# Kernel optimization log

Measured on AMD Instinct MI355X. Metric: run time of the kernel, lower is better.

The kernel has to match this reference:

```python
import jax, jax.numpy as jnp
import numpy as np

B, S, D, H, WINDOW = 2, 2048, 2048, 16, 256
HD = D // H  # head_dim = 128

def setup_inputs() -> dict:
    key = jax.random.key(0)
    ks = jax.random.split(key, 6)
    s = 0.02  # initializer_range-like scale for weights
    return {
        "hidden_states": jax.random.normal(ks[0], (B, S, D), jnp.float32),
        "attention_mask": jnp.ones((B, S), jnp.int32),
        "Wq": jax.random.normal(ks[1], (D, D), jnp.float32) * s,
        "Wk": jax.random.normal(ks[2], (D, D), jnp.float32) * s,
        "Wv": jax.random.normal(ks[3], (D, D), jnp.float32) * s,
        "Wo": jax.random.normal(ks[4], (D, D), jnp.float32) * s,
        "bo": jnp.zeros((D,), jnp.float32),
    }

def reference(hidden_states, attention_mask, Wq, Wk, Wv, Wo, bo):
    # GPT-Neo quirk: query is multiplied by sqrt(head_dim) and then
    # dot_product_attention_weights divides by sqrt(head_dim) -> net UNSCALED scores.
    q = (hidden_states @ Wq).reshape(B, S, H, HD)  # [B,S,H,hd]
    k = (hidden_states @ Wk).reshape(B, S, H, HD)
    v = (hidden_states @ Wv).reshape(B, S, H, HD)

    # local causal mask: attend iff i - window < j <= i
    i = jnp.arange(S)[:, None]
    j = jnp.arange(S)[None, :]
    local_causal = (j <= i) & (j > i - WINDOW)  # [S,S]
    mask = local_causal[None, None] & (attention_mask[:, None, None, :] > 0)  # [B,1,S,S]

    neg = jnp.finfo(jnp.float32).min
    scores = jnp.einsum("bqhd,bkhd->bhqk", q, k)  # [B,H,S,S] unscaled
    scores = jnp.where(mask, scores, neg)
    attn = jax.nn.softmax(scores, axis=-1)

    out = jnp.einsum("bhqk,bkhd->bqhd", attn, v).reshape(B, S, D)
    return out @ Wo + bo
```

## Files before the change

kernel.cpp:

```cpp
#include <hip/hip_runtime.h>

#define B_   2
#define S_   2048
#define D_   2048
#define H_   16
#define HD_  128
#define WIN_ 256
#define M_   (B_ * S_)

typedef float  f32x4  __attribute__((ext_vector_type(4)));
typedef short  s16x8  __attribute__((ext_vector_type(8)));
typedef __bf16 bf16x8 __attribute__((ext_vector_type(8)));
typedef unsigned short ushort_t;

__device__ inline unsigned short f2b(float f) {
  unsigned u = __builtin_bit_cast(unsigned, f);
  u += 0x7fffu + ((u >> 16) & 1u);
  return (unsigned short)(u >> 16);
}
__device__ inline float b2f(unsigned short h) {
  unsigned u = ((unsigned)h) << 16;
  return __builtin_bit_cast(float, u);
}

template <typename T>
__device__ auto mfma_impl(T a, T b, f32x4 c, int)
    -> decltype(__builtin_amdgcn_mfma_f32_16x16x32_bf16(a, b, c, 0, 0, 0)) {
  return __builtin_amdgcn_mfma_f32_16x16x32_bf16(a, b, c, 0, 0, 0);
}
template <typename T>
__device__ f32x4 mfma_impl(T a, T b, f32x4 c, long) {
  return __builtin_amdgcn_mfma_f32_16x16x32_bf16(
      __builtin_bit_cast(bf16x8, a), __builtin_bit_cast(bf16x8, b), c, 0, 0, 0);
}
__device__ inline f32x4 mfma_bf16(s16x8 a, s16x8 b, f32x4 c) {
  return mfma_impl(a, b, c, 0);
}

#if defined(__has_builtin)
#if __has_builtin(__builtin_amdgcn_global_load_lds)
#define HAS_GLL 1
#endif
#endif
#ifndef HAS_GLL
#define HAS_GLL 0
#endif

__device__ inline void gl_lds16(const ushort_t* g, ushort_t* lds_wave_base) {
#if HAS_GLL
  __builtin_amdgcn_global_load_lds(
      (const __attribute__((address_space(1))) unsigned int*)g,
      (__attribute__((address_space(3))) unsigned int*)lds_wave_base, 16, 0, 0);
#else
  const int lane = threadIdx.x & 63;
  *(uint4*)(lds_wave_base + lane * 8) = *(const uint4*)g;
#endif
}

__global__ __launch_bounds__(256) void k_split(const float* __restrict__ x,
                                               ushort_t* __restrict__ hi,
                                               ushort_t* __restrict__ lo, int n) {
  int i = (blockIdx.x * 256 + threadIdx.x) * 4;
  if (i + 3 < n) {
    float4 v = *(const float4*)(x + i);
    ushort4 h, l;
    h.x = f2b(v.x); l.x = f2b(v.x - b2f(h.x));
    h.y = f2b(v.y); l.y = f2b(v.y - b2f(h.y));
    h.z = f2b(v.z); l.z = f2b(v.z - b2f(h.z));
    h.w = f2b(v.w); l.w = f2b(v.w - b2f(h.w));
    *(ushort4*)(hi + i) = h;
    *(ushort4*)(lo + i) = l;
  }
}

__global__ __launch_bounds__(256) void k_transpose4(const float* __restrict__ W0,
                                                    const float* __restrict__ W1,
                                                    const float* __restrict__ W2,
                                                    const float* __restrict__ W3,
                                                    ushort_t* __restrict__ T0h,
                                                    ushort_t* __restrict__ T0l,
                                                    ushort_t* __restrict__ T1h,
                                                    ushort_t* __restrict__ T1l,
                                                    ushort_t* __restrict__ T2h,
                                                    ushort_t* __restrict__ T3h) {
  __shared__ float t[32][33];
  const int z = blockIdx.z;
  const float* W = (z == 0) ? W0 : (z == 1) ? W1 : (z == 2) ? W2 : W3;
  ushort_t* Th = (z == 0) ? T0h : (z == 1) ? T1h : (z == 2) ? T2h : T3h;
  ushort_t* Tl = (z == 0) ? T0l : (z == 1) ? T1l : nullptr;
  int bx = blockIdx.x * 32, by = blockIdx.y * 32;
  int tx = threadIdx.x, ty = threadIdx.y;
#pragma unroll
  for (int r = 0; r < 32; r += 8)
    t[ty + r][tx] = W[(size_t)(by + ty + r) * D_ + bx + tx];
  __syncthreads();
#pragma unroll
  for (int r = 0; r < 32; r += 8) {
    float v = t[tx][ty + r];
    unsigned short h = f2b(v);
    Th[(size_t)(bx + ty + r) * D_ + by + tx] = h;
    if (Tl) Tl[(size_t)(bx + ty + r) * D_ + by + tx] = f2b(v - b2f(h));
  }
}

__global__ __launch_bounds__(256) void k_vtrans(const ushort_t* __restrict__ Vb,
                                                ushort_t* __restrict__ Vt) {
  __shared__ ushort_t t[32][33];
  int bx = blockIdx.x * 32, by = blockIdx.y * 32, b = blockIdx.z;
  int tx = threadIdx.x, ty = threadIdx.y;
#pragma unroll
  for (int r = 0; r < 32; r += 8)
    t[ty + r][tx] = Vb[((size_t)(b * S_ + by + ty + r)) * D_ + bx + tx];
  __syncthreads();
#pragma unroll
  for (int r = 0; r < 32; r += 8)
    Vt[((size_t)(b * D_ + bx + ty + r)) * S_ + by + tx] = t[tx][ty + r];
}

template <int SPLIT, int OUT>
__global__ __launch_bounds__(256) void k_gemm(const ushort_t* __restrict__ Ah,
                                              const ushort_t* __restrict__ Al,
                                              const ushort_t* __restrict__ Bh,
                                              const ushort_t* __restrict__ Bl,
                                              ushort_t* __restrict__ Co,
                                              ushort_t* __restrict__ Col,
                                              float* __restrict__ Cf,
                                              const float* __restrict__ bias,
                                              int M, int N, int K) {
  constexpr int NA = (SPLIT >= 2) ? 2 : 1;
  constexpr int NBB = (SPLIT == 3) ? 2 : 1;
  __shared__ ushort_t Ash[NA][128][32];
  __shared__ ushort_t Bsh[NBB][128][32];
  const int tid = threadIdx.x;
  const int wave = tid >> 6, lane = tid & 63;
  const int m0 = blockIdx.y * 128, n0 = blockIdx.x * 128;
  const int wr = (wave >> 1) * 64, wc = (wave & 1) * 64;
  const int quad = lane >> 4, l16 = lane & 15;
  const int srow = tid >> 2, scol = (tid & 3) * 8;
  const size_t aoff = (size_t)(m0 + srow) * K + scol;
  const size_t boff = (size_t)(n0 + srow) * K + scol;
  const int wofs = wave * 512;

  f32x4 acc[4][4] = {};
  for (int k0 = 0; k0 < K; k0 += 32) {
    gl_lds16(Ah + aoff + k0,                  &Ash[0][0][0] + wofs);
    gl_lds16(Ah + aoff + k0 + (size_t)64 * K, &Ash[0][64][0] + wofs);
    if (SPLIT >= 2) {
      gl_lds16(Al + aoff + k0,                  &Ash[NA - 1][0][0] + wofs);
      gl_lds16(Al + aoff + k0 + (size_t)64 * K, &Ash[NA - 1][64][0] + wofs);
    }
    gl_lds16(Bh + boff + k0,                  &Bsh[0][0][0] + wofs);
    gl_lds16(Bh + boff + k0 + (size_t)64 * K, &Bsh[0][64][0] + wofs);
    if (SPLIT == 3) {
      gl_lds16(Bl + boff + k0,                  &Bsh[NBB - 1][0][0] + wofs);
      gl_lds16(Bl + boff + k0 + (size_t)64 * K, &Bsh[NBB - 1][64][0] + wofs);
    }
    __syncthreads();
    s16x8 bf[NBB][4];
#pragma unroll
    for (int s = 0; s < NBB; s++)
#pragma unroll
      for (int jt = 0; jt < 4; jt++)
        bf[s][jt] = *(const s16x8*)&Bsh[s][wc + jt * 16 + l16][quad * 8];
#pragma unroll
    for (int it = 0; it < 4; it++) {
      s16x8 ah = *(const s16x8*)&Ash[0][wr + it * 16 + l16][quad * 8];
      s16x8 al;
      if (SPLIT >= 2) al = *(const s16x8*)&Ash[NA - 1][wr + it * 16 + l16][quad * 8];
#pragma unroll
      for (int jt = 0; jt < 4; jt++) {
        acc[it][jt] = mfma_bf16(ah, bf[0][jt], acc[it][jt]);
        if (SPLIT == 3)
          acc[it][jt] = mfma_bf16(ah, bf[NBB - 1][jt], acc[it][jt]);
        if (SPLIT >= 2)
          acc[it][jt] = mfma_bf16(al, bf[0][jt], acc[it][jt]);
      }
    }
    __syncthreads();
  }
#pragma unroll
  for (int it = 0; it < 4; it++)
#pragma unroll
    for (int jt = 0; jt < 4; jt++)
#pragma unroll
      for (int r = 0; r < 4; r++) {
        int row = m0 + wr + it * 16 + quad * 4 + r;
        int col = n0 + wc + jt * 16 + l16;
        float v = acc[it][jt][r];
        if (OUT == 2) {
          Cf[(size_t)row * N + col] = v + bias[col];
        } else if (OUT == 1) {
          unsigned short h = f2b(v);
          Co[(size_t)row * N + col]  = h;
          Col[(size_t)row * N + col] = f2b(v - b2f(h));
        } else {
          Co[(size_t)row * N + col] = f2b(v);
        }
      }
}

__global__ __launch_bounds__(256) void k_fattn(const ushort_t* __restrict__ Qh,
                                               const ushort_t* __restrict__ Ql,
                                               const ushort_t* __restrict__ Kh,
                                               const ushort_t* __restrict__ Vt,
                                               const int* __restrict__ amask,
                                               ushort_t* __restrict__ AO) {
  __shared__ ushort_t Ksh[64][136];
  __shared__ ushort_t Vs[128][72];
  __shared__ ushort_t ps[4][16][72];
  __shared__ int ams[320];
  const int tid = threadIdx.x;
  const int wave = tid >> 6, lane = tid & 63;
  const int quad = lane >> 4, l16 = lane & 15;
  const int qt = blockIdx.x, h = blockIdx.y, b = blockIdx.z;
  const int q0 = qt * 64;

  for (int x = tid; x < 320; x += 256) {
    int j = q0 - 256 + x;
    ams[x] = (j >= 0) ? amask[b * S_ + j] : 0;
  }

  const int qrowA = q0 + wave * 16 + l16;
  const ushort_t* qbh = Qh + ((size_t)(b * S_ + qrowA) * D_) + h * HD_;
  const ushort_t* qbl = Ql + ((size_t)(b * S_ + qrowA) * D_) + h * HD_;
  s16x8 qh[4], ql[4];
#pragma unroll
  for (int kk = 0; kk < 4; kk++) {
    qh[kk] = *(const s16x8*)(qbh + kk * 32 + quad * 8);
    ql[kk] = *(const s16x8*)(qbl + kk * 32 + quad * 8);
  }

  f32x4 O[8] = {};
  float m_run[4], l_run[4];
#pragma unroll
  for (int r = 0; r < 4; r++) { m_run[r] = -3.0e38f; l_run[r] = 0.f; }

  const int t0 = (qt < 4) ? (4 - qt) : 0;
  for (int t = t0; t < 5; t++) {
    const int kb = q0 - 256 + 64 * t;
    __syncthreads();
    {
      const int key = tid >> 2, dimb = (tid & 3) * 32;
      const ushort_t* kgh = Kh + ((size_t)(b * S_ + kb + key) * D_) + h * HD_ + dimb;
#pragma unroll
      for (int u = 0; u < 4; u++)
        *(uint4*)&Ksh[key][dimb + u * 8] = *(const uint4*)(kgh + u * 8);
      const int hd = tid >> 1, keyb = (tid & 1) * 32;
      const ushort_t* vg = Vt + ((size_t)(b * D_ + h * HD_ + hd) * S_) + kb + keyb;
#pragma unroll
      for (int u = 0; u < 4; u++)
        *(uint4*)&Vs[hd][keyb + u * 8] = *(const uint4*)(vg + u * 8);
    }
    __syncthreads();

    f32x4 sacc[4] = {};
#pragma unroll
    for (int kk = 0; kk < 4; kk++)
#pragma unroll
      for (int nt = 0; nt < 4; nt++) {
        s16x8 kfh = *(const s16x8*)&Ksh[nt * 16 + l16][kk * 32 + quad * 8];
        sacc[nt] = mfma_bf16(qh[kk], kfh, sacc[nt]);
        sacc[nt] = mfma_bf16(ql[kk], kfh, sacc[nt]);
      }

#pragma unroll
    for (int nt = 0; nt < 4; nt++) {
      const int j = kb + nt * 16 + l16;
      const bool amok = ams[64 * t + nt * 16 + l16] != 0;
#pragma unroll
      for (int r = 0; r < 4; r++) {
        const int iq = q0 + wave * 16 + quad * 4 + r;
        const bool ok = amok && (j <= iq) && (j > iq - WIN_);
        if (!ok) sacc[nt][r] = -3.0e38f;
      }
    }
    float mt[4];
#pragma unroll
    for (int r = 0; r < 4; r++) {
      mt[r] = fmaxf(fmaxf(sacc[0][r], sacc[1][r]), fmaxf(sacc[2][r], sacc[3][r]));
      mt[r] = fmaxf(mt[r], __shfl_xor(mt[r], 1));
      mt[r] = fmaxf(mt[r], __shfl_xor(mt[r], 2));
      mt[r] = fmaxf(mt[r], __shfl_xor(mt[r], 4));
      mt[r] = fmaxf(mt[r], __shfl_xor(mt[r], 8));
    }
    float alpha[4], lt[4];
#pragma unroll
    for (int r = 0; r < 4; r++) {
      float mnew = fmaxf(m_run[r], mt[r]);
      alpha[r] = __expf(m_run[r] - mnew);
      m_run[r] = mnew;
      lt[r] = 0.f;
#pragma unroll
      for (int nt = 0; nt < 4; nt++) {
        float s = sacc[nt][r];
        float p = (s > -1.0e30f) ? __expf(s - mnew) : 0.f;
        sacc[nt][r] = p;
        lt[r] += p;
      }
      lt[r] += __shfl_xor(lt[r], 1);
      lt[r] += __shfl_xor(lt[r], 2);
      lt[r] += __shfl_xor(lt[r], 4);
      lt[r] += __shfl_xor(lt[r], 8);
      l_run[r] = l_run[r] * alpha[r] + lt[r];
    }
#pragma unroll
    for (int o = 0; o < 8; o++)
#pragma unroll
      for (int r = 0; r < 4; r++) O[o][r] *= alpha[r];
#pragma unroll
    for (int nt = 0; nt < 4; nt++)
#pragma unroll
      for (int r = 0; r < 4; r++)
        ps[wave][quad * 4 + r][nt * 16 + l16] = f2b(sacc[nt][r]);
    __syncthreads();
#pragma unroll
    for (int kk2 = 0; kk2 < 2; kk2++) {
      s16x8 pf = *(const s16x8*)&ps[wave][l16][kk2 * 32 + quad * 8];
#pragma unroll
      for (int o = 0; o < 8; o++) {
        s16x8 vf = *(const s16x8*)&Vs[o * 16 + l16][kk2 * 32 + quad * 8];
        O[o] = mfma_bf16(pf, vf, O[o]);
      }
    }
  }
#pragma unroll
  for (int r = 0; r < 4; r++) l_run[r] = 1.0f / l_run[r];
#pragma unroll
  for (int o = 0; o < 8; o++)
#pragma unroll
    for (int r = 0; r < 4; r++) {
      int row = q0 + wave * 16 + quad * 4 + r;
      AO[((size_t)(b * S_ + row) * D_) + h * HD_ + o * 16 + l16] = f2b(O[o][r] * l_run[r]);
    }
}

extern "C" void kernel_launch(void* const* d_in, const int* in_sizes, int n_in,
                              void* d_out, int out_size, void* d_ws, size_t ws_size,
                              hipStream_t stream) {
  const float* hs    = (const float*)d_in[0];
  const int*   amask = (const int*)d_in[1];
  const float* Wq    = (const float*)d_in[2];
  const float* Wk    = (const float*)d_in[3];
  const float* Wv    = (const float*)d_in[4];
  const float* Wo    = (const float*)d_in[5];
  const float* bo    = (const float*)d_in[6];
  float* out = (float*)d_out;

  char* p = (char*)d_ws;
  ushort_t* hsHi = (ushort_t*)p; p += (size_t)16 << 20;
  ushort_t* hsLo = (ushort_t*)p; p += (size_t)16 << 20;
  ushort_t* WqTh = (ushort_t*)p; p += (size_t)8 << 20;
  ushort_t* WqTl = (ushort_t*)p; p += (size_t)8 << 20;
  ushort_t* WkTh = (ushort_t*)p; p += (size_t)8 << 20;
  ushort_t* WkTl = (ushort_t*)p; p += (size_t)8 << 20;  (void)WkTl;
  ushort_t* WvTh = (ushort_t*)p; p += (size_t)8 << 20;
  ushort_t* WoTh = (ushort_t*)p; p += (size_t)8 << 20;
  ushort_t* Qhb  = (ushort_t*)p; p += (size_t)16 << 20;
  ushort_t* Qlb  = (ushort_t*)p; p += (size_t)16 << 20;
  ushort_t* Khb  = (ushort_t*)p; p += (size_t)16 << 20;
  ushort_t* Vb   = (ushort_t*)p; p += (size_t)16 << 20;
  ushort_t* Vt   = (ushort_t*)p; p += (size_t)16 << 20;

  k_split<<<M_ * D_ / 1024, 256, 0, stream>>>(hs, hsHi, hsLo, M_ * D_);
  dim3 tb(32, 8), tg4(D_ / 32, D_ / 32, 4);
  k_transpose4<<<tg4, tb, 0, stream>>>(Wq, Wk, Wv, Wo, WqTh, WqTl, WkTh, nullptr, WvTh, WoTh);

  dim3 gg(D_ / 128, M_ / 128);
  k_gemm<3, 1><<<gg, 256, 0, stream>>>(hsHi, hsLo, WqTh, WqTl, Qhb, Qlb, nullptr, nullptr, M_, D_, D_);
  k_gemm<2, 0><<<gg, 256, 0, stream>>>(hsHi, hsLo, WkTh, nullptr, Khb, nullptr, nullptr, nullptr, M_, D_, D_);
  k_gemm<1, 0><<<gg, 256, 0, stream>>>(hsHi, nullptr, WvTh, nullptr, Vb, nullptr, nullptr, nullptr, M_, D_, D_);

  dim3 vg(D_ / 32, S_ / 32, B_);
  k_vtrans<<<vg, tb, 0, stream>>>(Vb, Vt);

  dim3 ag(S_ / 64, H_, B_);
  k_fattn<<<ag, 256, 0, stream>>>(Qhb, Qlb, Khb, Vt, amask, hsHi );

  k_gemm<1, 2><<<gg, 256, 0, stream>>>(hsHi , nullptr, WoTh, nullptr, nullptr, nullptr, out, bo, M_, D_, D_);
}
```

Baseline: 494.8 us.

## Replace GEMM with 256x128-tile, triple-buffered, swizzled-LDS 8-wave kernel

Replaces the 128x128, 4-wave GEMM with a 512-thread kernel that computes a 256x128 tile using a 64-wide K step. Global-to-LDS staging is triple-buffered and overlapped with MFMA work through explicit waitcnt, barriers and setprio. The LDS layout uses an XOR swizzle to avoid bank conflicts. The split-precision products are now handled as extra K segments (hi*hi, lo*hi, hi*lo) with one MFMA per term instead of interleaving them per tile. The risks are higher LDS use, which lowers occupancy, and fewer blocks in the grid.

```diff
diff --git a/kernel.cpp b/kernel.cpp
--- a/kernel.cpp
+++ b/kernel.cpp
@@ -117,76 +117,135 @@
     Vt[((size_t)(b * D_ + bx + ty + r)) * S_ + by + tx] = t[tx][ty + r];
 }
 
-template <int SPLIT, int OUT>
-__global__ __launch_bounds__(256) void k_gemm(const ushort_t* __restrict__ Ah,
-                                              const ushort_t* __restrict__ Al,
-                                              const ushort_t* __restrict__ Bh,
-                                              const ushort_t* __restrict__ Bl,
-                                              ushort_t* __restrict__ Co,
-                                              ushort_t* __restrict__ Col,
-                                              float* __restrict__ Cf,
-                                              const float* __restrict__ bias,
-                                              int M, int N, int K) {
-  constexpr int NA = (SPLIT >= 2) ? 2 : 1;
-  constexpr int NBB = (SPLIT == 3) ? 2 : 1;
-  __shared__ ushort_t Ash[NA][128][32];
-  __shared__ ushort_t Bsh[NBB][128][32];
+
+__device__ inline void stage_chunk(const ushort_t* __restrict__ gbase, int K,
+                                   int rowbase, ushort_t* ldsTile, int tid) {
+  const int rr = tid >> 3;
+  const int gs = ((tid & 7) ^ (rr & 7)) * 8;
+  gl_lds16(gbase + (size_t)(rowbase + rr) * K + gs,
+           ldsTile + rowbase * 64 + (tid >> 6) * 512);
+}
+
+template <int NSEG, int OUT>
+__global__ __launch_bounds__(512) void k_gemm8(
+    const ushort_t* __restrict__ A0, const ushort_t* __restrict__ A1,
+    const ushort_t* __restrict__ A2, const ushort_t* __restrict__ B0,
+    const ushort_t* __restrict__ B2, ushort_t* __restrict__ Co,
+    ushort_t* __restrict__ Col, float* __restrict__ Cf,
+    const float* __restrict__ bias, int M, int N, int K) {
+  __shared__ ushort_t As_[3][256 * 64];
+  __shared__ ushort_t Bs_[3][128 * 64];
   const int tid = threadIdx.x;
   const int wave = tid >> 6, lane = tid & 63;
-  const int m0 = blockIdx.y * 128, n0 = blockIdx.x * 128;
-  const int wr = (wave >> 1) * 64, wc = (wave & 1) * 64;
   const int quad = lane >> 4, l16 = lane & 15;
-  const int srow = tid >> 2, scol = (tid & 3) * 8;
-  const size_t aoff = (size_t)(m0 + srow) * K + scol;
-  const size_t boff = (size_t)(n0 + srow) * K + scol;
-  const int wofs = wave * 512;
+  const int m0 = blockIdx.y * 256, n0 = blockIdx.x * 128;
+  const int wrM = (wave >> 1) * 64;
+  const int wcN = (wave & 1) * 64;
+  const int aRowB = (wrM + l16) * 64;
+  const int bRowB = (wcN + l16) * 64;
+  int ks8[2];
+  ks8[0] = ((0 + quad) ^ (l16 & 7)) * 8;
+  ks8[1] = ((4 + quad) ^ (l16 & 7)) * 8;
+  const int NT = NSEG * 32;
+
+  {
+    const ushort_t* Ab0 = A0 + (size_t)m0 * K;
+    const ushort_t* Bb0 = B0 + (size_t)n0 * K;
+#pragma unroll
+    for (int t = 0; t < 2; ++t) {
+      const ushort_t* Ab = Ab0 + t * 64;
+      const ushort_t* Bb = Bb0 + t * 64;
+      stage_chunk(Ab, K, 0,   &As_[t][0], tid);
+      stage_chunk(Ab, K, 64,  &As_[t][0], tid);
+      stage_chunk(Ab, K, 128, &As_[t][0], tid);
+      stage_chunk(Ab, K, 192, &As_[t][0], tid);
+      stage_chunk(Bb, K, 0,   &Bs_[t][0], tid);
+      stage_chunk(Bb, K, 64,  &Bs_[t][0], tid);
+    }
+  }
+  asm volatile("s_waitcnt vmcnt(6)" ::: "memory");
+  __builtin_amdgcn_s_barrier();
+  asm volatile("" ::: "memory");
 
   f32x4 acc[4][4] = {};
-  for (int k0 = 0; k0 < K; k0 += 32) {
-    gl_lds16(Ah + aoff + k0,                  &Ash[0][0][0] + wofs);
-    gl_lds16(Ah + aoff + k0 + (size_t)64 * K, &Ash[0][64][0] + wofs);
-    if (SPLIT >= 2) {
-      gl_lds16(Al + aoff + k0,                  &Ash[NA - 1][0][0] + wofs);
-      gl_lds16(Al + aoff + k0 + (size_t)64 * K, &Ash[NA - 1][64][0] + wofs);
-    }
-    gl_lds16(Bh + boff + k0,                  &Bsh[0][0][0] + wofs);
-    gl_lds16(Bh + boff + k0 + (size_t)64 * K, &Bsh[0][64][0] + wofs);
-    if (SPLIT == 3) {
-      gl_lds16(Bl + boff + k0,                  &Bsh[NBB - 1][0][0] + wofs);
-      gl_lds16(Bl + boff + k0 + (size_t)64 * K, &Bsh[NBB - 1][64][0] + wofs);
-    }
-    __syncthreads();
-    s16x8 bf[NBB][4];
-#pragma unroll
-    for (int s = 0; s < NBB; s++)
-#pragma unroll
-      for (int jt = 0; jt < 4; jt++)
-        bf[s][jt] = *(const s16x8*)&Bsh[s][wc + jt * 16 + l16][quad * 8];
-#pragma unroll
-    for (int it = 0; it < 4; it++) {
-      s16x8 ah = *(const s16x8*)&Ash[0][wr + it * 16 + l16][quad * 8];
-      s16x8 al;
-      if (SPLIT >= 2) al = *(const s16x8*)&Ash[NA - 1][wr + it * 16 + l16][quad * 8];
-#pragma unroll
-      for (int jt = 0; jt < 4; jt++) {
-        acc[it][jt] = mfma_bf16(ah, bf[0][jt], acc[it][jt]);
-        if (SPLIT == 3)
-          acc[it][jt] = mfma_bf16(ah, bf[NBB - 1][jt], acc[it][jt]);
-        if (SPLIT >= 2)
-          acc[it][jt] = mfma_bf16(al, bf[0][jt], acc[it][jt]);
-      }
-    }
-    __syncthreads();
-  }
-#pragma unroll
-  for (int it = 0; it < 4; it++)
-#pragma unroll
-    for (int jt = 0; jt < 4; jt++)
-#pragma unroll
-      for (int r = 0; r < 4; r++) {
-        int row = m0 + wr + it * 16 + quad * 4 + r;
-        int col = n0 + wc + jt * 16 + l16;
-        float v = acc[it][jt][r];
+  int cur = 0;
+  for (int kt = 0; kt < NT; ++kt) {
+    const int st = kt + 2;
+    const bool doStage = (st < NT);
+    int sbuf = cur + 2; if (sbuf >= 3) sbuf -= 3;
+    ushort_t* At  = &As_[cur][0];
+    ushort_t* Bt  = &Bs_[cur][0];
+    ushort_t* Ads = &As_[sbuf][0];
+    ushort_t* Bds = &Bs_[sbuf][0];
+    const ushort_t* Asb = A0;
+    const ushort_t* Bsb = B0;
+    if (doStage) {
+      const int sg = st >> 5;
+      const ushort_t* Ag = A0;
+      const ushort_t* Bg = B0;
+      if (NSEG >= 2 && sg == 1) Ag = A1;
+      if (NSEG == 3 && sg == 2) { Ag = A2; Bg = B2; }
+      Asb = Ag + (size_t)m0 * K + (size_t)(st & 31) * 64;
+      Bsb = Bg + (size_t)n0 * K + (size_t)(st & 31) * 64;
+    }
+    s16x8 bf[4][2];
+#pragma unroll
+    for (int p = 0; p < 2; ++p) {
+      s16x8 af[2][2];
+#pragma unroll
+      for (int i = 0; i < 2; ++i)
+#pragma unroll
+        for (int s = 0; s < 2; ++s)
+          af[i][s] = *(const s16x8*)(At + aRowB + (p * 2 + i) * 1024 + ks8[s]);
+      if (p == 0) {
+#pragma unroll
+        for (int nt = 0; nt < 4; ++nt)
+#pragma unroll
+          for (int s = 0; s < 2; ++s)
+            bf[nt][s] = *(const s16x8*)(Bt + bRowB + nt * 1024 + ks8[s]);
+      }
+      if (doStage) {
+        if (p == 0) {
+          stage_chunk(Asb, K, 0,   Ads, tid);
+          stage_chunk(Asb, K, 64,  Ads, tid);
+          stage_chunk(Asb, K, 128, Ads, tid);
+        } else {
+          stage_chunk(Asb, K, 192, Ads, tid);
+          stage_chunk(Bsb, K, 0,   Bds, tid);
+          stage_chunk(Bsb, K, 64,  Bds, tid);
+        }
+      }
+      __builtin_amdgcn_s_barrier();
+      asm volatile("s_waitcnt lgkmcnt(0)" ::: "memory");
+      __builtin_amdgcn_sched_barrier(0);
+      __builtin_amdgcn_s_setprio(1);
+#pragma unroll
+      for (int i = 0; i < 2; ++i)
+#pragma unroll
+        for (int nt = 0; nt < 4; ++nt)
+#pragma unroll
+          for (int s = 0; s < 2; ++s)
+            acc[p * 2 + i][nt] = mfma_bf16(af[i][s], bf[nt][s], acc[p * 2 + i][nt]);
+      __builtin_amdgcn_s_setprio(0);
+      if (p == 1) {
+        if (doStage) asm volatile("s_waitcnt vmcnt(6)" ::: "memory");
+        else         asm volatile("s_waitcnt vmcnt(0)" ::: "memory");
+      }
+      __builtin_amdgcn_s_barrier();
+      asm volatile("" ::: "memory");
+    }
+    cur = (cur == 2) ? 0 : cur + 1;
+  }
+
+#pragma unroll
+  for (int mt = 0; mt < 4; ++mt)
+#pragma unroll
+    for (int nt = 0; nt < 4; ++nt)
+#pragma unroll
+      for (int r = 0; r < 4; ++r) {
+        int row = m0 + wrM + mt * 16 + quad * 4 + r;
+        int col = n0 + wcN + nt * 16 + l16;
+        float v = acc[mt][nt][r];
         if (OUT == 2) {
           Cf[(size_t)row * N + col] = v + bias[col];
         } else if (OUT == 1) {
@@ -365,10 +424,13 @@
   dim3 tb(32, 8), tg4(D_ / 32, D_ / 32, 4);
   k_transpose4<<<tg4, tb, 0, stream>>>(Wq, Wk, Wv, Wo, WqTh, WqTl, WkTh, nullptr, WvTh, WoTh);
 
-  dim3 gg(D_ / 128, M_ / 128);
-  k_gemm<3, 1><<<gg, 256, 0, stream>>>(hsHi, hsLo, WqTh, WqTl, Qhb, Qlb, nullptr, nullptr, M_, D_, D_);
-  k_gemm<2, 0><<<gg, 256, 0, stream>>>(hsHi, hsLo, WkTh, nullptr, Khb, nullptr, nullptr, nullptr, M_, D_, D_);
-  k_gemm<1, 0><<<gg, 256, 0, stream>>>(hsHi, nullptr, WvTh, nullptr, Vb, nullptr, nullptr, nullptr, M_, D_, D_);
+  dim3 g8(D_ / 128, M_ / 256);
+  k_gemm8<3, 1><<<g8, 512, 0, stream>>>(hsHi, hsLo, hsHi, WqTh, WqTl,
+                                        Qhb, Qlb, nullptr, nullptr, M_, D_, D_);
+  k_gemm8<2, 0><<<g8, 512, 0, stream>>>(hsHi, hsLo, nullptr, WkTh, nullptr,
+                                        Khb, nullptr, nullptr, nullptr, M_, D_, D_);
+  k_gemm8<1, 0><<<g8, 512, 0, stream>>>(hsHi, nullptr, nullptr, WvTh, nullptr,
+                                        Vb, nullptr, nullptr, nullptr, M_, D_, D_);
 
   dim3 vg(D_ / 32, S_ / 32, B_);
   k_vtrans<<<vg, tb, 0, stream>>>(Vb, Vt);
@@ -376,5 +438,6 @@
   dim3 ag(S_ / 64, H_, B_);
   k_fattn<<<ag, 256, 0, stream>>>(Qhb, Qlb, Khb, Vt, amask, hsHi );
 
-  k_gemm<1, 2><<<gg, 256, 0, stream>>>(hsHi , nullptr, WoTh, nullptr, nullptr, nullptr, out, bo, M_, D_, D_);
-}
+  k_gemm8<1, 2><<<g8, 512, 0, stream>>>(hsHi , nullptr, nullptr, WoTh, nullptr,
+                                        nullptr, nullptr, out, bo, M_, D_, D_);
+}
```

After: 462.0 us. -6.6%, faster.
